# Kernel tuning notes

Hardware: AMD Instinct MI355X
Metric: run time of the kernel (lower is better)

## Reference

```python
import jax, jax.numpy as jnp
import numpy as np

P = 32  # window_size


def _window_x(x, p):
    # [b, c, n1*p, n2*p] -> [(b*n1*n2), c, p, p]
    b, c, h, w = x.shape
    n1, n2 = h // p, w // p
    x = x.reshape(b, c, n1, p, n2, p).transpose(0, 2, 4, 1, 3, 5)
    return x.reshape(b * n1 * n2, c, p, p)


def _window_v(v, p):
    # [b, c, n1*p, n2*p] -> [(b*n1*n2), p*p, c]
    b, c, h, w = v.shape
    n1, n2 = h // p, w // p
    v = v.reshape(b, c, n1, p, n2, p).transpose(0, 2, 4, 3, 5, 1)
    return v.reshape(b * n1 * n2, p * p, c)


def _unwindow(out, b, n1, n2, p):
    # [(b*n1*n2), p*p, c] -> [b, c, n1*p, n2*p]
    c = out.shape[-1]
    out = out.reshape(b, n1, n2, p, p, c).transpose(0, 5, 1, 3, 2, 4)
    return out.reshape(b, c, n1 * p, n2 * p)


def setup_inputs() -> dict:
    key = jax.random.key(0)
    k1, k2, k3 = jax.random.split(key, 3)
    x = jax.random.normal(k1, (32, 512, 64, 64), dtype=jnp.float32)
    v = jax.random.uniform(k2, (32, 15, 64, 64), dtype=jnp.float32)
    # 1x1 conv weight, bias-free: out=dim_in//2=256, in=512
    w_qk = jax.random.normal(k3, (256, 512), dtype=jnp.float32) * 0.02
    return {"x": x, "v": v, "w_qk": w_qk}


def reference(x, v, w_qk):
    b, c, h, w = x.shape
    p = P
    n1, n2 = h // p, w // p
    xw = _window_x(x, p)              # [BW, 512, p, p]
    vw = _window_v(v, p)              # [BW, p*p, 15]
    # 1x1 conv == channel matmul, then tokens-last layout [BW, p*p, 256]
    q = jnp.einsum('bnij,cn->bijc', xw, w_qk).reshape(xw.shape[0], p * p, -1)
    q = q / (jnp.linalg.norm(q, axis=-1, keepdims=True) + 1e-6)
    dots = jax.nn.relu(jnp.einsum('bik,bjk->bij', q, q))   # cosine sim, [BW, p^2, p^2]
    attn = dots / (jnp.sum(dots, axis=-1, keepdims=True) + 1e-6)
    out = jnp.einsum('bij,bjk->bik', attn, vw)              # [BW, p^2, 15]
    return _unwindow(out, b, n1, n2, p)
```

## Files before the change

kernel.cpp:

```cpp
#include <hip/hip_runtime.h>
#include <hip/hip_bf16.h>

typedef __attribute__((ext_vector_type(8))) short short8;
typedef __attribute__((ext_vector_type(4))) float f32x4;
typedef __attribute__((ext_vector_type(2))) float f32x2;
typedef __attribute__((ext_vector_type(4))) unsigned short ushort4v;
typedef __attribute__((ext_vector_type(2))) unsigned int uint32x2;

__device__ __forceinline__ unsigned short f2bf(float f) {
    __hip_bfloat16 h = __float2bfloat16(f);
    return __builtin_bit_cast(unsigned short, h);
}
__device__ __forceinline__ unsigned int pack2(float a, float b) {
    return (unsigned int)f2bf(a) | ((unsigned int)f2bf(b) << 16);
}
__device__ __forceinline__ unsigned int pk_fp8x4(float a0, float a1, float a2, float a3) {
    int v = 0;
    v = __builtin_amdgcn_cvt_pk_fp8_f32(a0, a1, v, false);
    v = __builtin_amdgcn_cvt_pk_fp8_f32(a2, a3, v, true);
    return (unsigned int)v;
}
__device__ __forceinline__ void gload_lds16(const void* g, void* l) {
    __builtin_amdgcn_global_load_lds((const __attribute__((address_space(1))) unsigned int*)g,
                                     (__attribute__((address_space(3))) unsigned int*)l, 16, 0, 0);
}

#define VMCNT(N) asm volatile("s_waitcnt vmcnt(" #N ")" ::: "memory")
#define LGKM0()  asm volatile("s_waitcnt lgkmcnt(0)" ::: "memory")

__global__ __launch_bounds__(256) void k0_wt(const float* __restrict__ w,
                                             unsigned short* __restrict__ wt) {
    int T = blockIdx.x * 256 + threadIdx.x;
    int c = T & 255, u = T >> 8;
    const float* s = w + c * 512 + u * 8;
    f32x4 a = *(const f32x4*)s;
    f32x4 b = *(const f32x4*)(s + 4);
    short8 o;
    o[0] = (short)f2bf(a[0]); o[1] = (short)f2bf(a[1]);
    o[2] = (short)f2bf(a[2]); o[3] = (short)f2bf(a[3]);
    o[4] = (short)f2bf(b[0]); o[5] = (short)f2bf(b[1]);
    o[6] = (short)f2bf(b[2]); o[7] = (short)f2bf(b[3]);
    size_t off = (size_t)(((u * 256 + c) * 16) ^ ((u & 3) << 4));
    *(short8*)((char*)wt + off) = o;
}

__global__ __launch_bounds__(256, 2) void k1_qgemm(const float* __restrict__ x,
                                                   const unsigned short* __restrict__ wt,
                                                   unsigned char* __restrict__ qn) {
    const int blk = blockIdx.x;
    const int b_  = blk >> 5;
    const int wh  = (blk >> 4) & 1;
    const int rb  = blk & 15;
    const int winbase = b_ * 4 + wh * 2;

    __shared__ __align__(16) char smem[65536];

    const int tid  = threadIdx.x;
    const int lane = tid & 63;
    const int wv   = tid >> 6;
    const int lo   = lane & 15;
    const int hi   = lane >> 4;

    f32x4 acc[4][8];
#pragma unroll
    for (int mi = 0; mi < 4; ++mi)
#pragma unroll
        for (int ni = 0; ni < 8; ++ni) acc[mi][ni] = (f32x4){0.f, 0.f, 0.f, 0.f};

    const float* xslab = x + (size_t)b_ * 512 * 4096 + (size_t)(wh * 32 + rb * 2) * 64;
    const int tq = tid & 31;
    const int cs = tid >> 5;
    const float* xpbase = xslab + (size_t)(cs * 4) * 4096 + tq * 4;

    f32x4 bregs[4];

#define K1_ISSUE_A(KT, BUF)                                                        \
    {                                                                              \
        const char* src_ = (const char*)wt + (size_t)(KT) * 16384;                 \
        char* dst_ = smem + (BUF) * 16384;                                         \
        _Pragma("unroll")                                                          \
        for (int r_ = 0; r_ < 4; ++r_) {                                           \
            int idx_ = (r_ * 256 + tid) * 16;                                      \
            gload_lds16(src_ + idx_, dst_ + idx_);                                 \
        }                                                                          \
    }
#define K1_LOAD_B(KT)                                                              \
    {                                                                              \
        const float* xp_ = xpbase + (size_t)(KT) * 32 * 4096;                      \
        _Pragma("unroll")                                                          \
        for (int c_ = 0; c_ < 4; ++c_) bregs[c_] = *(const f32x4*)(xp_ + (size_t)c_ * 4096); \
    }
#define K1_WRITE_B(BUF)                                                            \
    {                                                                              \
        char* lb_ = smem + 32768 + (BUF) * 10240;                                  \
        _Pragma("unroll")                                                          \
        for (int e_ = 0; e_ < 4; ++e_) {                                           \
            ushort4v u_ = {f2bf(bregs[0][e_]), f2bf(bregs[1][e_]),                 \
                           f2bf(bregs[2][e_]), f2bf(bregs[3][e_])};                \
            *(ushort4v*)(lb_ + (tq * 4 + e_) * 80 + cs * 8) = u_;                  \
        }                                                                          \
    }

    K1_ISSUE_A(0, 0);
    K1_LOAD_B(0);
    K1_WRITE_B(0);
    K1_LOAD_B(1);
    LGKM0();
    __builtin_amdgcn_s_barrier();

    for (int kt = 0; kt < 16; ++kt) {
        const int b = kt & 1;
        {
            const int ktn = (kt + 1 < 16) ? kt + 1 : 15;
            K1_ISSUE_A(ktn, b ^ 1);
        }
        short8 af[4], bfr[8];
#pragma unroll
        for (int mi = 0; mi < 4; ++mi) {
            int base = (hi * 256 + wv * 64 + mi * 16 + lo) * 16;
            af[mi] = *(const short8*)(smem + b * 16384 + (base ^ ((hi & 3) << 4)));
        }
#pragma unroll
        for (int ni = 0; ni < 8; ++ni)
            bfr[ni] = *(const short8*)(smem + 32768 + b * 10240 + (ni * 16 + lo) * 80 + hi * 16);
        __builtin_amdgcn_s_setprio(1);
#pragma unroll
        for (int mi = 0; mi < 4; ++mi)
#pragma unroll
            for (int ni = 0; ni < 8; ++ni)
                acc[mi][ni] = __builtin_amdgcn_mfma_f32_16x16x32_bf16(af[mi], bfr[ni], acc[mi][ni], 0, 0, 0);
        __builtin_amdgcn_s_setprio(0);
        K1_WRITE_B(b ^ 1);
        __builtin_amdgcn_sched_barrier(0);
        {
            const int ktn2 = (kt + 2 < 16) ? kt + 2 : 15;
            K1_LOAD_B(ktn2);
        }
        VMCNT(4);
        LGKM0();
        __builtin_amdgcn_s_barrier();
    }
    VMCNT(0);

    float part[8];
#pragma unroll
    for (int ni = 0; ni < 8; ++ni) {
        float s = 0.f;
#pragma unroll
        for (int mi = 0; mi < 4; ++mi)
#pragma unroll
            for (int r = 0; r < 4; ++r) s += acc[mi][ni][r] * acc[mi][ni][r];
        s += __shfl_xor(s, 16);
        s += __shfl_xor(s, 32);
        part[ni] = s;
    }
    if (hi == 0) {
#pragma unroll
        for (int ni = 0; ni < 8; ++ni)
            *(float*)(smem + 53248 + (wv * 128 + ni * 16 + lo) * 4) = part[ni];
    }
    __syncthreads();

    float inv[8];
#pragma unroll
    for (int ni = 0; ni < 8; ++ni) {
        const int tl = ni * 16 + lo;
        float s = *(const float*)(smem + 53248 + (0 * 128 + tl) * 4)
                + *(const float*)(smem + 53248 + (1 * 128 + tl) * 4)
                + *(const float*)(smem + 53248 + (2 * 128 + tl) * 4)
                + *(const float*)(smem + 53248 + (3 * 128 + tl) * 4);
        inv[ni] = 1.f / (sqrtf(s) + 1e-6f);
    }

#pragma unroll
    for (int ni = 0; ni < 8; ++ni) {
        const int f    = ni * 16 + lo;
        const int swzf = (f & 3) << 4;
#pragma unroll
        for (int mi = 0; mi < 4; ++mi) {
            const int c = wv * 64 + mi * 16 + hi * 4;
            unsigned int u = pk_fp8x4(acc[mi][ni][0] * inv[ni], acc[mi][ni][1] * inv[ni],
                                      acc[mi][ni][2] * inv[ni], acc[mi][ni][3] * inv[ni]);
            *(unsigned int*)(smem + f * 256 + (c ^ swzf)) = u;
        }
    }
    __syncthreads();

#pragma unroll
    for (int it = 0; it < 8; ++it) {
        const int unit = it * 256 + tid;
        const int f    = unit >> 4;
        const int c16  = (unit & 15) * 16;
        f32x4 d = *(const f32x4*)(smem + f * 256 + (c16 ^ ((f & 3) << 4)));
        const int ww  = (f >> 5) & 1;
        const int rho = f >> 6;
        const int rq  = rb * 64 + rho * 32 + (f & 31);
        char* qw = (char*)qn + (size_t)(winbase + ww) * (1024 * 256);
        *(f32x4*)(qw + (size_t)rq * 256 + (c16 ^ ((rq & 3) << 4))) = d;
    }
}

__global__ __launch_bounds__(256, 2) void k2_attn(const unsigned char* __restrict__ qn,
                                                  const float* __restrict__ v,
                                                  float* __restrict__ out) {
    const int g   = blockIdx.x;
    const int win = g & 127;
    const int qb  = g >> 7;
    const int b_  = win >> 2;
    const int h0  = ((win >> 1) & 1) << 5;
    const int w0  = (win & 1) << 5;

    __shared__ __align__(16) char lK[64 * 256];
    __shared__ __align__(16) unsigned short lP[256][72];
    __shared__ __align__(16) unsigned short lV[16][72];

    const int tid  = threadIdx.x;
    const int lane = tid & 63;
    const int wv   = tid >> 6;
    const int lo   = lane & 15;
    const int hi   = lane >> 4;

    const unsigned char* qwin = qn + (size_t)win * (1024 * 256);
    const int qw0 = qb * 256 + wv * 64;

    long qa8[4][8];
#pragma unroll
    for (int mi = 0; mi < 4; ++mi) {
        const int rq = qw0 + mi * 16 + lo;
        const size_t swz = (size_t)((rq & 3) << 4);
#pragma unroll
        for (int kc = 0; kc < 8; ++kc)
            qa8[mi][kc] = *(const long*)(qwin + (((size_t)rq * 256 + kc * 32 + hi * 8) ^ swz));
    }

    f32x4 accout[4];
#pragma unroll
    for (int t = 0; t < 4; ++t) accout[t] = (f32x4){0.f, 0.f, 0.f, 0.f};

    const float* vbase = v + (size_t)b_ * 15 * 4096 + (size_t)h0 * 64 + w0;
    char* lKb = (char*)lK;
    char* lPb = (char*)&lP[0][0];
    char* lVb = (char*)&lV[0][0];

    for (int chk = 0; chk < 16; ++chk) {
        const int kbase = chk << 6;
        __syncthreads();
        {
            const char* src = (const char*)qwin + (size_t)kbase * 256;
#pragma unroll
            for (int r = 0; r < 4; ++r) {
                int idx = (r * 256 + tid) * 16;
                gload_lds16(src + idx, lKb + idx);
            }
        }
        {
            const int chn = tid & 15;
            const int kp  = tid >> 4;
            uint32x2 u;
            if (chn < 15) {
                int jk = kbase + kp * 4;
                const float* vp = vbase + (size_t)chn * 4096 + ((jk >> 5) * 64 + (jk & 31));
                f32x4 d = *(const f32x4*)vp;
                u[0] = pack2(d[0], d[1]);
                u[1] = pack2(d[2], d[3]);
            } else {
                u[0] = 0x3F803F80u;
                u[1] = 0x3F803F80u;
            }
            *(uint32x2*)(lVb + chn * 144 + kp * 8) = u;
        }
        __syncthreads();

#pragma unroll
        for (int ni = 0; ni < 4; ++ni) {
            f32x4 st[4];
#pragma unroll
            for (int mi = 0; mi < 4; ++mi) st[mi] = (f32x4){0.f, 0.f, 0.f, 0.f};
            __builtin_amdgcn_s_setprio(1);
#pragma unroll
            for (int kc = 0; kc < 8; ++kc) {
                const int row = ni * 16 + lo;
                const int off = ((row * 256) + kc * 32 + hi * 8) ^ ((row & 3) << 4);
                long kb = *(const long*)(lKb + off);
#pragma unroll
                for (int mi = 0; mi < 4; ++mi)
                    st[mi] = __builtin_amdgcn_mfma_f32_16x16x32_fp8_fp8(kb, qa8[mi][kc], st[mi], 0, 0, 0);
            }
            __builtin_amdgcn_s_setprio(0);
#pragma unroll
            for (int mi = 0; mi < 4; ++mi) {
                uint32x2 u;
                u[0] = pack2(fmaxf(st[mi][0], 0.f), fmaxf(st[mi][1], 0.f));
                u[1] = pack2(fmaxf(st[mi][2], 0.f), fmaxf(st[mi][3], 0.f));
                *(uint32x2*)(lPb + (wv * 64 + mi * 16 + lo) * 144 + ni * 32 + hi * 8) = u;
            }
        }

        __builtin_amdgcn_s_setprio(1);
#pragma unroll
        for (int t = 0; t < 4; ++t) {
#pragma unroll
            for (int ks = 0; ks < 2; ++ks) {
                short8 pa  = *(const short8*)(lPb + (wv * 64 + t * 16 + lo) * 144 + ks * 64 + hi * 16);
                short8 vbf = *(const short8*)(lVb + lo * 144 + ks * 64 + hi * 16);
                accout[t] = __builtin_amdgcn_mfma_f32_16x16x32_bf16(pa, vbf, accout[t], 0, 0, 0);
            }
        }
        __builtin_amdgcn_s_setprio(0);
    }

#pragma unroll
    for (int t = 0; t < 4; ++t) {
#pragma unroll
        for (int r = 0; r < 4; ++r) {
            float rs = __shfl(accout[t][r], (lane & 48) | 15);
            if (lo < 15) {
                int q = qw0 + t * 16 + hi * 4 + r;
                out[(size_t)(b_ * 15 + lo) * 4096 + (size_t)(h0 + (q >> 5)) * 64 + (w0 + (q & 31))] =
                    accout[t][r] / (rs + 1e-6f);
            }
        }
    }
}

extern "C" void kernel_launch(void* const* d_in, const int* in_sizes, int n_in,
                              void* d_out, int out_size, void* d_ws, size_t ws_size,
                              hipStream_t stream) {
    const float* x = (const float*)d_in[0];
    const float* v = (const float*)d_in[1];
    const float* w = (const float*)d_in[2];
    float* out = (float*)d_out;

    unsigned char*  qn = (unsigned char*)d_ws;
    unsigned short* wt = (unsigned short*)((char*)d_ws + (size_t)32 * 1024 * 1024);

    k0_wt<<<64, 256, 0, stream>>>(w, wt);
    k1_qgemm<<<1024, 256, 0, stream>>>(x, wt, qn);
    k2_attn<<<512, 256, 0, stream>>>(qn, v, out);
}
```

Measured before the change: 126.0 us.

## Double-buffer K and V tiles in attention kernel with prefetch pipelining

Splits the K and V shared-memory tiles into two buffers each. The next K chunk is issued through global_load_lds and the V chunk is register-prefetched two iterations ahead while the current chunk is computed. The two __syncthreads per iteration become one manual vmcnt/lgkmcnt wait plus a barrier. This is meant to hide global memory latency behind the MFMA work, at the cost of more LDS per block, which could reduce occupancy, and of fragile hand-written wait counts.

```diff
diff --git a/kernel.cpp b/kernel.cpp
--- a/kernel.cpp
+++ b/kernel.cpp
@@ -210,9 +210,9 @@
     const int h0  = ((win >> 1) & 1) << 5;
     const int w0  = (win & 1) << 5;
 
-    __shared__ __align__(16) char lK[64 * 256];
+    __shared__ __align__(16) char lK[2][64 * 256];
     __shared__ __align__(16) unsigned short lP[256][72];
-    __shared__ __align__(16) unsigned short lV[16][72];
+    __shared__ __align__(16) unsigned short lV[2][16][72];
 
     const int tid  = threadIdx.x;
     const int lane = tid & 63;
@@ -238,39 +238,56 @@
     for (int t = 0; t < 4; ++t) accout[t] = (f32x4){0.f, 0.f, 0.f, 0.f};
 
     const float* vbase = v + (size_t)b_ * 15 * 4096 + (size_t)h0 * 64 + w0;
-    char* lKb = (char*)lK;
+    const int chn = tid & 15;
+    const int kp  = tid >> 4;
+    const float* vch = vbase + (size_t)(chn < 15 ? chn : 14) * 4096;
     char* lPb = (char*)&lP[0][0];
-    char* lVb = (char*)&lV[0][0];
+
+#define K2_VADDR(CHK) (vch + ((((CHK) * 64 + kp * 4) >> 5) * 64 + (((CHK) * 64 + kp * 4) & 31)))
+#define K2_WRITE_V(BUF, D)                                                         \
+    {                                                                              \
+        uint32x2 u_;                                                               \
+        if (chn < 15) { u_[0] = pack2((D)[0], (D)[1]); u_[1] = pack2((D)[2], (D)[3]); } \
+        else          { u_[0] = 0x3F803F80u;           u_[1] = 0x3F803F80u; }      \
+        *(uint32x2*)((char*)lV[BUF] + chn * 144 + kp * 8) = u_;                    \
+    }
+#define K2_ISSUE_K(CHK, BUF)                                                       \
+    {                                                                              \
+        const char* src_ = (const char*)qwin + (size_t)(CHK) * 16384;              \
+        char* dst_ = (char*)lK[BUF];                                               \
+        _Pragma("unroll")                                                          \
+        for (int r_ = 0; r_ < 4; ++r_) {                                           \
+            int idx_ = (r_ * 256 + tid) * 16;                                      \
+            gload_lds16(src_ + idx_, dst_ + idx_);                                 \
+        }                                                                          \
+    }
+
+    f32x4 vpre;
+    {
+        f32x4 d0 = *(const f32x4*)K2_VADDR(0);
+        K2_WRITE_V(0, d0);
+    }
+    K2_ISSUE_K(0, 0);
+    vpre = *(const f32x4*)K2_VADDR(1);
+    VMCNT(1);
+    LGKM0();
+    __builtin_amdgcn_s_barrier();
 
     for (int chk = 0; chk < 16; ++chk) {
-        const int kbase = chk << 6;
-        __syncthreads();
+        const int b = chk & 1;
         {
-            const char* src = (const char*)qwin + (size_t)kbase * 256;
-#pragma unroll
-            for (int r = 0; r < 4; ++r) {
-                int idx = (r * 256 + tid) * 16;
-                gload_lds16(src + idx, lKb + idx);
-            }
-        }
+            const int cn = (chk + 1 < 16) ? chk + 1 : 15;
+            K2_ISSUE_K(cn, b ^ 1);
+        }
+        K2_WRITE_V(b ^ 1, vpre);
+        __builtin_amdgcn_sched_barrier(0);
         {
-            const int chn = tid & 15;
-            const int kp  = tid >> 4;
-            uint32x2 u;
-            if (chn < 15) {
-                int jk = kbase + kp * 4;
-                const float* vp = vbase + (size_t)chn * 4096 + ((jk >> 5) * 64 + (jk & 31));
-                f32x4 d = *(const f32x4*)vp;
-                u[0] = pack2(d[0], d[1]);
-                u[1] = pack2(d[2], d[3]);
-            } else {
-                u[0] = 0x3F803F80u;
-                u[1] = 0x3F803F80u;
-            }
-            *(uint32x2*)(lVb + chn * 144 + kp * 8) = u;
-        }
-        __syncthreads();
-
+            const int cv = (chk + 2 < 16) ? chk + 2 : 15;
+            vpre = *(const f32x4*)K2_VADDR(cv);
+        }
+        __builtin_amdgcn_sched_barrier(0);
+
+        const char* lKb = (const char*)lK[b];
 #pragma unroll
         for (int ni = 0; ni < 4; ++ni) {
             f32x4 st[4];
@@ -295,19 +312,23 @@
                 *(uint32x2*)(lPb + (wv * 64 + mi * 16 + lo) * 144 + ni * 32 + hi * 8) = u;
             }
         }
-
         __builtin_amdgcn_s_setprio(1);
 #pragma unroll
         for (int t = 0; t < 4; ++t) {
 #pragma unroll
             for (int ks = 0; ks < 2; ++ks) {
                 short8 pa  = *(const short8*)(lPb + (wv * 64 + t * 16 + lo) * 144 + ks * 64 + hi * 16);
-                short8 vbf = *(const short8*)(lVb + lo * 144 + ks * 64 + hi * 16);
+                short8 vbf = *(const short8*)((const char*)lV[b] + lo * 144 + ks * 64 + hi * 16);
                 accout[t] = __builtin_amdgcn_mfma_f32_16x16x32_bf16(pa, vbf, accout[t], 0, 0, 0);
             }
         }
         __builtin_amdgcn_s_setprio(0);
-    }
+
+        VMCNT(1);
+        LGKM0();
+        __builtin_amdgcn_s_barrier();
+    }
+    VMCNT(0);
 
 #pragma unroll
     for (int t = 0; t < 4; ++t) {
```

After: 126.1 us. About the same (+0.1%).
